# Optimization experiments

Hardware: AMD Instinct MI355X
Metric: run time of the kernel (lower is better)

The kernel has to match this reference:

```python
import jax, jax.numpy as jnp
import numpy as np

N_EMBD = 1024
N_HEAD = 16

def setup_inputs() -> dict:
    key = jax.random.key(0)
    ks = jax.random.split(key, 5)
    x = jax.random.normal(ks[0], (4, 2048, N_EMBD), dtype=jnp.float32)
    # torch Linear default init ~ U(-1/sqrt(fan_in), 1/sqrt(fan_in)); use scaled normals
    s = 1.0 / np.sqrt(N_EMBD)
    W_attn = jax.random.normal(ks[1], (N_EMBD, 3 * N_EMBD), dtype=jnp.float32) * s
    b_attn = jax.random.normal(ks[2], (3 * N_EMBD,), dtype=jnp.float32) * s
    W_proj = jax.random.normal(ks[3], (N_EMBD, N_EMBD), dtype=jnp.float32) * s
    b_proj = jax.random.normal(ks[4], (N_EMBD,), dtype=jnp.float32) * s
    return {"x": x, "W_attn": W_attn, "b_attn": b_attn, "W_proj": W_proj, "b_proj": b_proj}

def reference(x, W_attn, b_attn, W_proj, b_proj) -> jnp.ndarray:
    B, T, C = x.shape
    H = N_HEAD
    D = C // H  # head dim
    qkv = x @ W_attn + b_attn  # [B,T,3C]
    q, k, v = jnp.split(qkv, 3, axis=-1)
    # [B,T,C] -> [B,H,T,D]
    q = q.reshape(B, T, H, D).transpose(0, 2, 1, 3)
    k = k.reshape(B, T, H, D).transpose(0, 2, 1, 3)
    v = v.reshape(B, T, H, D).transpose(0, 2, 1, 3)
    scale = 1.0 / jnp.sqrt(jnp.float32(D))
    att = jnp.einsum('bhqd,bhkd->bhqk', q, k) * scale  # [B,H,T,T]
    causal = jnp.tril(jnp.ones((T, T), dtype=bool))
    att = jnp.where(causal[None, None, :, :], att, -jnp.inf)
    att = jax.nn.softmax(att, axis=-1)
    y = jnp.einsum('bhqk,bhkd->bhqd', att, v)  # [B,H,T,D]
    y = y.transpose(0, 2, 1, 3).reshape(B, T, C)
    return y @ W_proj + b_proj
```

## Files before the change

kernel.cpp:

```cpp
#include <hip/hip_runtime.h>
#include <stdint.h>


typedef __attribute__((ext_vector_type(8))) short short8;
typedef __attribute__((ext_vector_type(4))) float floatx4;

#define AS1C(p) ((const __attribute__((address_space(1))) void*)(p))
#define AS3(p)  ((__attribute__((address_space(3))) void*)(p))

#define SC2F 0.18033688011f

__device__ __forceinline__ unsigned short f2bf(float f) {
  unsigned int u = __builtin_bit_cast(unsigned int, f);
  u = (u + 0x7fffu + ((u >> 16) & 1u)) >> 16;
  return (unsigned short)u;
}
__device__ __forceinline__ unsigned short f2bf_trunc(float f) {
  return (unsigned short)(__builtin_bit_cast(unsigned int, f) >> 16);
}

__global__ void k_cvt(const float* __restrict__ in, unsigned short* __restrict__ out, int n4) {
  int i = blockIdx.x * blockDim.x + threadIdx.x;
  if (i < n4) {
    float4 v = ((const float4*)in)[i];
    ushort4 o;
    o.x = f2bf(v.x); o.y = f2bf(v.y); o.z = f2bf(v.z); o.w = f2bf(v.w);
    ((ushort4*)out)[i] = o;
  }
}

__global__ void k_tw(const float* __restrict__ in, unsigned short* __restrict__ out, int K, int N) {
  __shared__ float t[32][33];
  int n0 = blockIdx.x * 32, k0 = blockIdx.y * 32;
  int tx = threadIdx.x, ty = threadIdx.y;
#pragma unroll
  for (int i = 0; i < 4; i++)
    t[ty + 8 * i][tx] = in[(size_t)(k0 + ty + 8 * i) * N + n0 + tx];
  __syncthreads();
#pragma unroll
  for (int i = 0; i < 4; i++)
    out[(size_t)(n0 + ty + 8 * i) * K + k0 + tx] = f2bf(t[tx][ty + 8 * i]);
}

__global__ void k_tv(const unsigned short* __restrict__ qkv, unsigned short* __restrict__ vt) {
  __shared__ unsigned short t[32][33];
  int t0 = blockIdx.x * 32;
  int d0 = blockIdx.y * 32;
  int bh = blockIdx.z;
  int b = bh >> 4, h = bh & 15;
  int tx = threadIdx.x, ty = threadIdx.y;
#pragma unroll
  for (int i = 0; i < 4; i++)
    t[ty + 8 * i][tx] = qkv[(size_t)(b * 2048 + t0 + ty + 8 * i) * 3072 + 2048 + h * 64 + d0 + tx];
  __syncthreads();
#pragma unroll
  for (int i = 0; i < 4; i++)
    vt[(size_t)(bh * 64 + d0 + ty + 8 * i) * 2048 + t0 + tx] = t[tx][ty + 8 * i];
}

template <int OUT_F32>
__global__ __launch_bounds__(256)
void k_gemm(const unsigned short* __restrict__ A,
            const unsigned short* __restrict__ Bt,
            const float* __restrict__ bias,
            void* __restrict__ Cout, int M, int N, int K, int NX) {
  __shared__ unsigned short lA[128 * 64];
  __shared__ unsigned short lB[128 * 64];
  int lin = blockIdx.x;
  int xcd = lin & 7, idx = lin >> 3;
  int bx = idx % NX;
  int by = xcd + 8 * (idx / NX);
  int tid = threadIdx.x;
  int lane = tid & 63, wv = tid >> 6;
  int lc = lane & 15, quad = lane >> 4;
  int m0 = by * 128, n0 = bx * 128;
  int wm = (wv >> 1) * 64, wn = (wv & 1) * 64;
  int sw = lc & 7;

  floatx4 acc[4][4];
#pragma unroll
  for (int i = 0; i < 4; i++)
#pragma unroll
    for (int j = 0; j < 4; j++) acc[i][j] = (floatx4){0.f, 0.f, 0.f, 0.f};

  int srow = tid >> 3;
  int scol = (((tid & 7) ^ (srow & 7))) * 8;
  const unsigned short* gA = A + (size_t)(m0 + srow) * K + scol;
  const unsigned short* gB = Bt + (size_t)(n0 + srow) * K + scol;

  for (int k0 = 0; k0 < K; k0 += 64) {
#pragma unroll
    for (int c = 0; c < 4; c++) {
      __builtin_amdgcn_global_load_lds(AS1C(gA + (size_t)(32 * c) * K + k0),
                                       AS3(lA + (32 * c + 8 * wv) * 64), 16, 0, 0);
      __builtin_amdgcn_global_load_lds(AS1C(gB + (size_t)(32 * c) * K + k0),
                                       AS3(lB + (32 * c + 8 * wv) * 64), 16, 0, 0);
    }
    __syncthreads();
#pragma unroll
    for (int s = 0; s < 2; s++) {
      short8 af[4], bfr[4];
#pragma unroll
      for (int i = 0; i < 4; i++)
        af[i] = *(const short8*)(lA + (wm + i * 16 + lc) * 64 + (((s * 4 + quad) ^ sw) * 8));
#pragma unroll
      for (int j = 0; j < 4; j++)
        bfr[j] = *(const short8*)(lB + (wn + j * 16 + lc) * 64 + (((s * 4 + quad) ^ sw) * 8));
#pragma unroll
      for (int i = 0; i < 4; i++)
#pragma unroll
        for (int j = 0; j < 4; j++)
          acc[i][j] = __builtin_amdgcn_mfma_f32_16x16x32_bf16(af[i], bfr[j], acc[i][j], 0, 0, 0);
    }
    __syncthreads();
  }

  float bv[4];
#pragma unroll
  for (int j = 0; j < 4; j++) bv[j] = bias[n0 + wn + j * 16 + lc];
#pragma unroll
  for (int i = 0; i < 4; i++) {
#pragma unroll
    for (int j = 0; j < 4; j++) {
      float sc = (!OUT_F32 && (n0 + wn + j * 16) < 1024) ? SC2F : 1.0f;
#pragma unroll
      for (int r = 0; r < 4; r++) {
        size_t idx2 = (size_t)(m0 + wm + i * 16 + quad * 4 + r) * N + (n0 + wn + j * 16 + lc);
        float v = (acc[i][j][r] + bv[j]) * sc;
        if (OUT_F32) ((float*)Cout)[idx2] = v;
        else         ((unsigned short*)Cout)[idx2] = f2bf(v);
      }
    }
  }
}

#define LP_STRIDE 68
__global__ __launch_bounds__(256, 4)
void k_flash(const unsigned short* __restrict__ qkv,
             const unsigned short* __restrict__ vt,
             unsigned short* __restrict__ y) {
  __shared__ unsigned short lK[64 * 64];
  __shared__ unsigned short lVT[64 * 64];
  __shared__ unsigned short lP[4][2][16 * LP_STRIDE];
  int tid = threadIdx.x, lane = tid & 63, wv = tid >> 6;
  int lc = lane & 15, quad = lane >> 4;
  int sw = lc & 7;
  int lin = blockIdx.x;
  int xcd = lin & 7, idx = lin >> 3;
  int j   = idx & 15;
  int bh  = xcd + 8 * (idx >> 4);
  int b = bh >> 4, h = bh & 15;
  int qtA = j, qtB = 31 - j;
  int qrA = qtA * 64 + wv * 16;
  int qrB = qtB * 64 + wv * 16;

  short8 qfA[2], qfB[2];
  {
    const unsigned short* qp = qkv + (size_t)(b * 2048 + qrA + lc) * 3072 + h * 64 + quad * 8;
    qfA[0] = *(const short8*)qp;
    qfA[1] = *(const short8*)(qp + 32);
  }
  {
    const unsigned short* qp = qkv + (size_t)(b * 2048 + qrB + lc) * 3072 + h * 64 + quad * 8;
    qfB[0] = *(const short8*)qp;
    qfB[1] = *(const short8*)(qp + 32);
  }

  float rsA[4] = {0.f, 0.f, 0.f, 0.f}, rsB[4] = {0.f, 0.f, 0.f, 0.f};
  floatx4 oA[4], oB[4];
#pragma unroll
  for (int dt = 0; dt < 4; dt++) {
    oA[dt] = (floatx4){0.f, 0.f, 0.f, 0.f};
    oB[dt] = (floatx4){0.f, 0.f, 0.f, 0.f};
  }

  int srow = tid >> 3;
  int scol = ((tid & 7) ^ (srow & 7)) * 8;
  const unsigned short* gK = qkv + (size_t)(b * 2048 + srow) * 3072 + 1024 + h * 64 + scol;
  const unsigned short* gV = vt + (size_t)(bh * 64 + srow) * 2048 + scol;

  int nt = qtB + 1;

  for (int kv = 0; kv < nt; kv++) {
    int kv0 = kv * 64;
#pragma unroll
    for (int c = 0; c < 2; c++) {
      __builtin_amdgcn_global_load_lds(AS1C(gK + (size_t)(kv0 + 32 * c) * 3072),
                                       AS3(lK + (32 * c + 8 * wv) * 64), 16, 0, 0);
      __builtin_amdgcn_global_load_lds(AS1C(gV + (size_t)(32 * c) * 2048 + kv0),
                                       AS3(lVT + (32 * c + 8 * wv) * 64), 16, 0, 0);
    }
    __syncthreads();

    bool withA = (kv <= qtA);

    floatx4 sB[4], sA[4];
#pragma unroll
    for (int n = 0; n < 4; n++) {
      short8 kf0 = *(const short8*)(lK + (n * 16 + lc) * 64 + ((quad ^ sw) * 8));
      short8 kf1 = *(const short8*)(lK + (n * 16 + lc) * 64 + (((4 + quad) ^ sw) * 8));
      floatx4 t = (floatx4){0.f, 0.f, 0.f, 0.f};
      t = __builtin_amdgcn_mfma_f32_16x16x32_bf16(qfB[0], kf0, t, 0, 0, 0);
      t = __builtin_amdgcn_mfma_f32_16x16x32_bf16(qfB[1], kf1, t, 0, 0, 0);
      sB[n] = t;
      if (withA) {
        floatx4 u = (floatx4){0.f, 0.f, 0.f, 0.f};
        u = __builtin_amdgcn_mfma_f32_16x16x32_bf16(qfA[0], kf0, u, 0, 0, 0);
        u = __builtin_amdgcn_mfma_f32_16x16x32_bf16(qfA[1], kf1, u, 0, 0, 0);
        sA[n] = u;
      }
    }

    {
      bool diag = (kv == qtB);
#pragma unroll
      for (int n = 0; n < 4; n++)
#pragma unroll
        for (int r = 0; r < 4; r++) {
          float arg = sB[n][r];
          if (diag && (kv0 + n * 16 + lc > qrB + quad * 4 + r)) arg = -__builtin_inff();
          float p = __builtin_amdgcn_exp2f(arg);
          rsB[r] += p;
          lP[wv][0][(quad * 4 + r) * LP_STRIDE + n * 16 + lc] = f2bf_trunc(p);
        }
    }
    if (withA) {
      bool diag = (kv == qtA);
#pragma unroll
      for (int n = 0; n < 4; n++)
#pragma unroll
        for (int r = 0; r < 4; r++) {
          float arg = sA[n][r];
          if (diag && (kv0 + n * 16 + lc > qrA + quad * 4 + r)) arg = -__builtin_inff();
          float p = __builtin_amdgcn_exp2f(arg);
          rsA[r] += p;
          lP[wv][1][(quad * 4 + r) * LP_STRIDE + n * 16 + lc] = f2bf_trunc(p);
        }
    }

#pragma unroll
    for (int s2 = 0; s2 < 2; s2++) {
      short8 pfB = *(const short8*)(&lP[wv][0][0] + lc * LP_STRIDE + s2 * 32 + quad * 8);
      short8 pfA;
      if (withA) pfA = *(const short8*)(&lP[wv][1][0] + lc * LP_STRIDE + s2 * 32 + quad * 8);
#pragma unroll
      for (int dt = 0; dt < 4; dt++) {
        short8 vf = *(const short8*)(lVT + (dt * 16 + lc) * 64 + (((s2 * 4 + quad) ^ sw) * 8));
        oB[dt] = __builtin_amdgcn_mfma_f32_16x16x32_bf16(pfB, vf, oB[dt], 0, 0, 0);
        if (withA) oA[dt] = __builtin_amdgcn_mfma_f32_16x16x32_bf16(pfA, vf, oA[dt], 0, 0, 0);
      }
    }
    __syncthreads();
  }

#pragma unroll
  for (int off = 1; off < 16; off <<= 1)
#pragma unroll
    for (int r = 0; r < 4; r++) {
      rsA[r] += __shfl_xor(rsA[r], off);
      rsB[r] += __shfl_xor(rsB[r], off);
    }
#pragma unroll
  for (int r = 0; r < 4; r++) {
    float invA = 1.0f / rsA[r];
    float invB = 1.0f / rsB[r];
#pragma unroll
    for (int dt = 0; dt < 4; dt++) {
      size_t ia = (size_t)(b * 2048 + qrA + quad * 4 + r) * 1024 + h * 64 + dt * 16 + lc;
      size_t ib = (size_t)(b * 2048 + qrB + quad * 4 + r) * 1024 + h * 64 + dt * 16 + lc;
      y[ia] = f2bf(oA[dt][r] * invA);
      y[ib] = f2bf(oB[dt][r] * invB);
    }
  }
}

extern "C" void kernel_launch(void* const* d_in, const int* in_sizes, int n_in,
                              void* d_out, int out_size, void* d_ws, size_t ws_size,
                              hipStream_t stream) {
  const float* x      = (const float*)d_in[0];
  const float* W_attn = (const float*)d_in[1];
  const float* b_attn = (const float*)d_in[2];
  const float* W_proj = (const float*)d_in[3];
  const float* b_proj = (const float*)d_in[4];

  char* ws = (char*)d_ws;
  unsigned short* xb     = (unsigned short*)ws;
  unsigned short* wattnT = (unsigned short*)(ws + 16777216);
  unsigned short* wprojT = (unsigned short*)(ws + 23068672);
  unsigned short* qkv    = (unsigned short*)(ws + 25165824);
  unsigned short* vt     = (unsigned short*)(ws + 75497472);
  unsigned short* y      = xb;

  k_cvt<<<8192, 256, 0, stream>>>(x, xb, 8388608 / 4);
  k_tw<<<dim3(96, 32), dim3(32, 8), 0, stream>>>(W_attn, wattnT, 1024, 3072);
  k_tw<<<dim3(32, 32), dim3(32, 8), 0, stream>>>(W_proj, wprojT, 1024, 1024);
  k_gemm<0><<<24 * 64, 256, 0, stream>>>(xb, wattnT, b_attn, qkv, 8192, 3072, 1024, 24);
  k_tv<<<dim3(64, 2, 64), dim3(32, 8), 0, stream>>>(qkv, vt);
  k_flash<<<1024, 256, 0, stream>>>(qkv, vt, y);
  k_gemm<1><<<8 * 64, 256, 0, stream>>>(y, wprojT, b_proj, d_out, 8192, 1024, 1024, 8);
}
```

Measured before the change: 283.6 us.

## Process four causal-balanced query tiles per flash block sharing K/V loads

Each flash-attention block now handles four query tiles (j, 15-j, 16+j, 31-j) instead of two, so every K/V tile staged in LDS feeds up to four query tiles. This halves the grid to 512 blocks and drops the XCD-aware block remapping in favour of a plain 2D grid. The goal is to cut redundant K/V global loads and barrier overhead per unit of work. In exchange it raises register pressure (four sets of accumulators, with the occupancy hint removed), doubles the P scratch in LDS, and leaves fewer blocks to fill the CUs.

```diff
diff --git a/kernel.cpp b/kernel.cpp
--- a/kernel.cpp
+++ b/kernel.cpp
@@ -135,51 +135,46 @@
 }
 
 #define LP_STRIDE 68
-__global__ __launch_bounds__(256, 4)
+__global__ __launch_bounds__(256)
 void k_flash(const unsigned short* __restrict__ qkv,
              const unsigned short* __restrict__ vt,
              unsigned short* __restrict__ y) {
   __shared__ unsigned short lK[64 * 64];
   __shared__ unsigned short lVT[64 * 64];
-  __shared__ unsigned short lP[4][2][16 * LP_STRIDE];
+  __shared__ unsigned short lP[4][4][16 * LP_STRIDE];
   int tid = threadIdx.x, lane = tid & 63, wv = tid >> 6;
   int lc = lane & 15, quad = lane >> 4;
   int sw = lc & 7;
-  int lin = blockIdx.x;
-  int xcd = lin & 7, idx = lin >> 3;
-  int j   = idx & 15;
-  int bh  = xcd + 8 * (idx >> 4);
+  int j  = blockIdx.x;
+  int bh = blockIdx.y;
   int b = bh >> 4, h = bh & 15;
-  int qtA = j, qtB = 31 - j;
-  int qrA = qtA * 64 + wv * 16;
-  int qrB = qtB * 64 + wv * 16;
-
-  short8 qfA[2], qfB[2];
-  {
-    const unsigned short* qp = qkv + (size_t)(b * 2048 + qrA + lc) * 3072 + h * 64 + quad * 8;
-    qfA[0] = *(const short8*)qp;
-    qfA[1] = *(const short8*)(qp + 32);
-  }
-  {
-    const unsigned short* qp = qkv + (size_t)(b * 2048 + qrB + lc) * 3072 + h * 64 + quad * 8;
-    qfB[0] = *(const short8*)qp;
-    qfB[1] = *(const short8*)(qp + 32);
-  }
-
-  float rsA[4] = {0.f, 0.f, 0.f, 0.f}, rsB[4] = {0.f, 0.f, 0.f, 0.f};
-  floatx4 oA[4], oB[4];
-#pragma unroll
-  for (int dt = 0; dt < 4; dt++) {
-    oA[dt] = (floatx4){0.f, 0.f, 0.f, 0.f};
-    oB[dt] = (floatx4){0.f, 0.f, 0.f, 0.f};
-  }
+  int qt[4] = {j, 15 - j, 16 + j, 31 - j};
+
+  short8 qf[4][2];
+#pragma unroll
+  for (int t = 0; t < 4; t++) {
+    const unsigned short* qp =
+        qkv + (size_t)(b * 2048 + qt[t] * 64 + wv * 16 + lc) * 3072 + h * 64 + quad * 8;
+    qf[t][0] = *(const short8*)qp;
+    qf[t][1] = *(const short8*)(qp + 32);
+  }
+
+  float rs[4][4];
+  floatx4 o[4][4];
+#pragma unroll
+  for (int t = 0; t < 4; t++)
+#pragma unroll
+    for (int r = 0; r < 4; r++) {
+      rs[t][r] = 0.f;
+      o[t][r] = (floatx4){0.f, 0.f, 0.f, 0.f};
+    }
 
   int srow = tid >> 3;
   int scol = ((tid & 7) ^ (srow & 7)) * 8;
   const unsigned short* gK = qkv + (size_t)(b * 2048 + srow) * 3072 + 1024 + h * 64 + scol;
   const unsigned short* gV = vt + (size_t)(bh * 64 + srow) * 2048 + scol;
 
-  int nt = qtB + 1;
+  int nt = 32 - j;
 
   for (int kv = 0; kv < nt; kv++) {
     int kv0 = kv * 64;
@@ -192,86 +187,68 @@
     }
     __syncthreads();
 
-    bool withA = (kv <= qtA);
-
-    floatx4 sB[4], sA[4];
 #pragma unroll
     for (int n = 0; n < 4; n++) {
       short8 kf0 = *(const short8*)(lK + (n * 16 + lc) * 64 + ((quad ^ sw) * 8));
       short8 kf1 = *(const short8*)(lK + (n * 16 + lc) * 64 + (((4 + quad) ^ sw) * 8));
-      floatx4 t = (floatx4){0.f, 0.f, 0.f, 0.f};
-      t = __builtin_amdgcn_mfma_f32_16x16x32_bf16(qfB[0], kf0, t, 0, 0, 0);
-      t = __builtin_amdgcn_mfma_f32_16x16x32_bf16(qfB[1], kf1, t, 0, 0, 0);
-      sB[n] = t;
-      if (withA) {
-        floatx4 u = (floatx4){0.f, 0.f, 0.f, 0.f};
-        u = __builtin_amdgcn_mfma_f32_16x16x32_bf16(qfA[0], kf0, u, 0, 0, 0);
-        u = __builtin_amdgcn_mfma_f32_16x16x32_bf16(qfA[1], kf1, u, 0, 0, 0);
-        sA[n] = u;
-      }
-    }
-
-    {
-      bool diag = (kv == qtB);
-#pragma unroll
-      for (int n = 0; n < 4; n++)
-#pragma unroll
-        for (int r = 0; r < 4; r++) {
-          float arg = sB[n][r];
-          if (diag && (kv0 + n * 16 + lc > qrB + quad * 4 + r)) arg = -__builtin_inff();
-          float p = __builtin_amdgcn_exp2f(arg);
-          rsB[r] += p;
-          lP[wv][0][(quad * 4 + r) * LP_STRIDE + n * 16 + lc] = f2bf_trunc(p);
+#pragma unroll
+      for (int t = 0; t < 4; t++) {
+        if (kv <= qt[t]) {
+          floatx4 s = (floatx4){0.f, 0.f, 0.f, 0.f};
+          s = __builtin_amdgcn_mfma_f32_16x16x32_bf16(qf[t][0], kf0, s, 0, 0, 0);
+          s = __builtin_amdgcn_mfma_f32_16x16x32_bf16(qf[t][1], kf1, s, 0, 0, 0);
+          bool diag = (kv == qt[t]);
+#pragma unroll
+          for (int r = 0; r < 4; r++) {
+            float arg = s[r];
+            if (diag && (n * 16 + lc > wv * 16 + quad * 4 + r)) arg = -__builtin_inff();
+            float p = __builtin_amdgcn_exp2f(arg);
+            rs[t][r] += p;
+            lP[wv][t][(quad * 4 + r) * LP_STRIDE + n * 16 + lc] = f2bf_trunc(p);
+          }
         }
-    }
-    if (withA) {
-      bool diag = (kv == qtA);
-#pragma unroll
-      for (int n = 0; n < 4; n++)
-#pragma unroll
-        for (int r = 0; r < 4; r++) {
-          float arg = sA[n][r];
-          if (diag && (kv0 + n * 16 + lc > qrA + quad * 4 + r)) arg = -__builtin_inff();
-          float p = __builtin_amdgcn_exp2f(arg);
-          rsA[r] += p;
-          lP[wv][1][(quad * 4 + r) * LP_STRIDE + n * 16 + lc] = f2bf_trunc(p);
+      }
+    }
+
+#pragma unroll
+    for (int s2 = 0; s2 < 2; s2++) {
+      short8 vf[4];
+#pragma unroll
+      for (int dt = 0; dt < 4; dt++)
+        vf[dt] = *(const short8*)(lVT + (dt * 16 + lc) * 64 + (((s2 * 4 + quad) ^ sw) * 8));
+#pragma unroll
+      for (int t = 0; t < 4; t++) {
+        if (kv <= qt[t]) {
+          short8 pf = *(const short8*)(&lP[wv][t][0] + lc * LP_STRIDE + s2 * 32 + quad * 8);
+#pragma unroll
+          for (int dt = 0; dt < 4; dt++)
+            o[t][dt] = __builtin_amdgcn_mfma_f32_16x16x32_bf16(pf, vf[dt], o[t][dt], 0, 0, 0);
         }
-    }
-
-#pragma unroll
-    for (int s2 = 0; s2 < 2; s2++) {
-      short8 pfB = *(const short8*)(&lP[wv][0][0] + lc * LP_STRIDE + s2 * 32 + quad * 8);
-      short8 pfA;
-      if (withA) pfA = *(const short8*)(&lP[wv][1][0] + lc * LP_STRIDE + s2 * 32 + quad * 8);
+      }
+    }
+    __syncthreads();
+  }
+
+#pragma unroll
+  for (int off = 1; off < 16; off <<= 1)
+#pragma unroll
+    for (int t = 0; t < 4; t++)
+#pragma unroll
+      for (int r = 0; r < 4; r++)
+        rs[t][r] += __shfl_xor(rs[t][r], off);
+
+#pragma unroll
+  for (int t = 0; t < 4; t++)
+#pragma unroll
+    for (int r = 0; r < 4; r++) {
+      float inv = 1.0f / rs[t][r];
 #pragma unroll
       for (int dt = 0; dt < 4; dt++) {
-        short8 vf = *(const short8*)(lVT + (dt * 16 + lc) * 64 + (((s2 * 4 + quad) ^ sw) * 8));
-        oB[dt] = __builtin_amdgcn_mfma_f32_16x16x32_bf16(pfB, vf, oB[dt], 0, 0, 0);
-        if (withA) oA[dt] = __builtin_amdgcn_mfma_f32_16x16x32_bf16(pfA, vf, oA[dt], 0, 0, 0);
-      }
-    }
-    __syncthreads();
-  }
-
-#pragma unroll
-  for (int off = 1; off < 16; off <<= 1)
-#pragma unroll
-    for (int r = 0; r < 4; r++) {
-      rsA[r] += __shfl_xor(rsA[r], off);
-      rsB[r] += __shfl_xor(rsB[r], off);
-    }
-#pragma unroll
-  for (int r = 0; r < 4; r++) {
-    float invA = 1.0f / rsA[r];
-    float invB = 1.0f / rsB[r];
-#pragma unroll
-    for (int dt = 0; dt < 4; dt++) {
-      size_t ia = (size_t)(b * 2048 + qrA + quad * 4 + r) * 1024 + h * 64 + dt * 16 + lc;
-      size_t ib = (size_t)(b * 2048 + qrB + quad * 4 + r) * 1024 + h * 64 + dt * 16 + lc;
-      y[ia] = f2bf(oA[dt][r] * invA);
-      y[ib] = f2bf(oB[dt][r] * invB);
-    }
-  }
+        size_t ia = (size_t)(b * 2048 + qt[t] * 64 + wv * 16 + quad * 4 + r) * 1024
+                    + h * 64 + dt * 16 + lc;
+        y[ia] = f2bf(o[t][dt][r] * inv);
+      }
+    }
 }
 
 extern "C" void kernel_launch(void* const* d_in, const int* in_sizes, int n_in,
@@ -296,6 +273,6 @@
   k_tw<<<dim3(32, 32), dim3(32, 8), 0, stream>>>(W_proj, wprojT, 1024, 1024);
   k_gemm<0><<<24 * 64, 256, 0, stream>>>(xb, wattnT, b_attn, qkv, 8192, 3072, 1024, 24);
   k_tv<<<dim3(64, 2, 64), dim3(32, 8), 0, stream>>>(qkv, vt);
-  k_flash<<<1024, 256, 0, stream>>>(qkv, vt, y);
+  k_flash<<<dim3(8, 64), 256, 0, stream>>>(qkv, vt, y);
   k_gemm<1><<<8 * 64, 256, 0, stream>>>(y, wprojT, b_proj, d_out, 8192, 1024, 1024, 8);
 }
```

Result: faster. 274.4 us (-3.2%).

## Keep softmax probabilities in registers via transposed QK^T MFMA, drop LDS P staging

Applied to the files above, without the earlier changes.

The flash kernel now computes S^T by swapping the MFMA operands (K as A, Q as B). Each lane then holds four consecutive key positions for one query, which can be packed directly into a bf16 operand for 16x16x16 MFMAs in the PV product. This removes the per-wave LDS round-trip for P and its writes and reads, and simplifies row-sum reduction to two shuffles. It also swaps the XCD-aware 1D block swizzle for a plain 2D grid, which may change L2 locality across XCDs.

```diff
diff --git a/kernel.cpp b/kernel.cpp
--- a/kernel.cpp
+++ b/kernel.cpp
@@ -3,7 +3,9 @@
 
 
 typedef __attribute__((ext_vector_type(8))) short short8;
+typedef __attribute__((ext_vector_type(4))) short short4v;
 typedef __attribute__((ext_vector_type(4))) float floatx4;
+typedef __attribute__((ext_vector_type(2))) unsigned int uint2v;
 
 #define AS1C(p) ((const __attribute__((address_space(1))) void*)(p))
 #define AS3(p)  ((__attribute__((address_space(3))) void*)(p))
@@ -14,9 +16,6 @@
   unsigned int u = __builtin_bit_cast(unsigned int, f);
   u = (u + 0x7fffu + ((u >> 16) & 1u)) >> 16;
   return (unsigned short)u;
-}
-__device__ __forceinline__ unsigned short f2bf_trunc(float f) {
-  return (unsigned short)(__builtin_bit_cast(unsigned int, f) >> 16);
 }
 
 __global__ void k_cvt(const float* __restrict__ in, unsigned short* __restrict__ out, int n4) {
@@ -134,21 +133,17 @@
   }
 }
 
-#define LP_STRIDE 68
 __global__ __launch_bounds__(256, 4)
 void k_flash(const unsigned short* __restrict__ qkv,
              const unsigned short* __restrict__ vt,
              unsigned short* __restrict__ y) {
   __shared__ unsigned short lK[64 * 64];
   __shared__ unsigned short lVT[64 * 64];
-  __shared__ unsigned short lP[4][2][16 * LP_STRIDE];
   int tid = threadIdx.x, lane = tid & 63, wv = tid >> 6;
   int lc = lane & 15, quad = lane >> 4;
   int sw = lc & 7;
-  int lin = blockIdx.x;
-  int xcd = lin & 7, idx = lin >> 3;
-  int j   = idx & 15;
-  int bh  = xcd + 8 * (idx >> 4);
+  int j  = blockIdx.x;
+  int bh = blockIdx.y;
   int b = bh >> 4, h = bh & 15;
   int qtA = j, qtB = 31 - j;
   int qrA = qtA * 64 + wv * 16;
@@ -166,7 +161,7 @@
     qfB[1] = *(const short8*)(qp + 32);
   }
 
-  float rsA[4] = {0.f, 0.f, 0.f, 0.f}, rsB[4] = {0.f, 0.f, 0.f, 0.f};
+  float rsA = 0.f, rsB = 0.f;
   floatx4 oA[4], oB[4];
 #pragma unroll
   for (int dt = 0; dt < 4; dt++) {
@@ -193,84 +188,76 @@
     __syncthreads();
 
     bool withA = (kv <= qtA);
-
-    floatx4 sB[4], sA[4];
+    bool diagA = (kv == qtA), diagB = (kv == qtB);
+
+    short4v pfB[4], pfA[4];
 #pragma unroll
     for (int n = 0; n < 4; n++) {
       short8 kf0 = *(const short8*)(lK + (n * 16 + lc) * 64 + ((quad ^ sw) * 8));
       short8 kf1 = *(const short8*)(lK + (n * 16 + lc) * 64 + (((4 + quad) ^ sw) * 8));
-      floatx4 t = (floatx4){0.f, 0.f, 0.f, 0.f};
-      t = __builtin_amdgcn_mfma_f32_16x16x32_bf16(qfB[0], kf0, t, 0, 0, 0);
-      t = __builtin_amdgcn_mfma_f32_16x16x32_bf16(qfB[1], kf1, t, 0, 0, 0);
-      sB[n] = t;
+      {
+        floatx4 s = (floatx4){0.f, 0.f, 0.f, 0.f};
+        s = __builtin_amdgcn_mfma_f32_16x16x32_bf16(kf0, qfB[0], s, 0, 0, 0);
+        s = __builtin_amdgcn_mfma_f32_16x16x32_bf16(kf1, qfB[1], s, 0, 0, 0);
+        unsigned pu[4];
+#pragma unroll
+        for (int r = 0; r < 4; r++) {
+          float arg = s[r];
+          if (diagB && (n * 16 + quad * 4 + r > wv * 16 + lc)) arg = -__builtin_inff();
+          float p = __builtin_amdgcn_exp2f(arg);
+          rsB += p;
+          pu[r] = __builtin_bit_cast(unsigned, p);
+        }
+        uint2v pk = {(pu[0] >> 16) | (pu[1] & 0xffff0000u),
+                     (pu[2] >> 16) | (pu[3] & 0xffff0000u)};
+        pfB[n] = __builtin_bit_cast(short4v, pk);
+      }
       if (withA) {
-        floatx4 u = (floatx4){0.f, 0.f, 0.f, 0.f};
-        u = __builtin_amdgcn_mfma_f32_16x16x32_bf16(qfA[0], kf0, u, 0, 0, 0);
-        u = __builtin_amdgcn_mfma_f32_16x16x32_bf16(qfA[1], kf1, u, 0, 0, 0);
-        sA[n] = u;
-      }
-    }
-
-    {
-      bool diag = (kv == qtB);
-#pragma unroll
-      for (int n = 0; n < 4; n++)
+        floatx4 s = (floatx4){0.f, 0.f, 0.f, 0.f};
+        s = __builtin_amdgcn_mfma_f32_16x16x32_bf16(kf0, qfA[0], s, 0, 0, 0);
+        s = __builtin_amdgcn_mfma_f32_16x16x32_bf16(kf1, qfA[1], s, 0, 0, 0);
+        unsigned pu[4];
 #pragma unroll
         for (int r = 0; r < 4; r++) {
-          float arg = sB[n][r];
-          if (diag && (kv0 + n * 16 + lc > qrB + quad * 4 + r)) arg = -__builtin_inff();
+          float arg = s[r];
+          if (diagA && (n * 16 + quad * 4 + r > wv * 16 + lc)) arg = -__builtin_inff();
           float p = __builtin_amdgcn_exp2f(arg);
-          rsB[r] += p;
-          lP[wv][0][(quad * 4 + r) * LP_STRIDE + n * 16 + lc] = f2bf_trunc(p);
+          rsA += p;
+          pu[r] = __builtin_bit_cast(unsigned, p);
         }
-    }
-    if (withA) {
-      bool diag = (kv == qtA);
-#pragma unroll
-      for (int n = 0; n < 4; n++)
-#pragma unroll
-        for (int r = 0; r < 4; r++) {
-          float arg = sA[n][r];
-          if (diag && (kv0 + n * 16 + lc > qrA + quad * 4 + r)) arg = -__builtin_inff();
-          float p = __builtin_amdgcn_exp2f(arg);
-          rsA[r] += p;
-          lP[wv][1][(quad * 4 + r) * LP_STRIDE + n * 16 + lc] = f2bf_trunc(p);
-        }
-    }
-
-#pragma unroll
-    for (int s2 = 0; s2 < 2; s2++) {
-      short8 pfB = *(const short8*)(&lP[wv][0][0] + lc * LP_STRIDE + s2 * 32 + quad * 8);
-      short8 pfA;
-      if (withA) pfA = *(const short8*)(&lP[wv][1][0] + lc * LP_STRIDE + s2 * 32 + quad * 8);
+        uint2v pk = {(pu[0] >> 16) | (pu[1] & 0xffff0000u),
+                     (pu[2] >> 16) | (pu[3] & 0xffff0000u)};
+        pfA[n] = __builtin_bit_cast(short4v, pk);
+      }
+    }
+
+#pragma unroll
+    for (int n = 0; n < 4; n++) {
 #pragma unroll
       for (int dt = 0; dt < 4; dt++) {
-        short8 vf = *(const short8*)(lVT + (dt * 16 + lc) * 64 + (((s2 * 4 + quad) ^ sw) * 8));
-        oB[dt] = __builtin_amdgcn_mfma_f32_16x16x32_bf16(pfB, vf, oB[dt], 0, 0, 0);
-        if (withA) oA[dt] = __builtin_amdgcn_mfma_f32_16x16x32_bf16(pfA, vf, oA[dt], 0, 0, 0);
-      }
-    }
-    __syncthreads();
-  }
-
-#pragma unroll
-  for (int off = 1; off < 16; off <<= 1)
-#pragma unroll
-    for (int r = 0; r < 4; r++) {
-      rsA[r] += __shfl_xor(rsA[r], off);
-      rsB[r] += __shfl_xor(rsB[r], off);
-    }
-#pragma unroll
-  for (int r = 0; r < 4; r++) {
-    float invA = 1.0f / rsA[r];
-    float invB = 1.0f / rsB[r];
-#pragma unroll
-    for (int dt = 0; dt < 4; dt++) {
-      size_t ia = (size_t)(b * 2048 + qrA + quad * 4 + r) * 1024 + h * 64 + dt * 16 + lc;
-      size_t ib = (size_t)(b * 2048 + qrB + quad * 4 + r) * 1024 + h * 64 + dt * 16 + lc;
-      y[ia] = f2bf(oA[dt][r] * invA);
-      y[ib] = f2bf(oB[dt][r] * invB);
-    }
+        short4v vf = *(const short4v*)(lVT + (dt * 16 + lc) * 64 +
+                                       (((2 * n + (quad >> 1)) ^ sw) * 8) + (quad & 1) * 4);
+        oB[dt] = __builtin_amdgcn_mfma_f32_16x16x16bf16_1k(vf, pfB[n], oB[dt], 0, 0, 0);
+        if (withA)
+          oA[dt] = __builtin_amdgcn_mfma_f32_16x16x16bf16_1k(vf, pfA[n], oA[dt], 0, 0, 0);
+      }
+    }
+    __syncthreads();
+  }
+
+  rsA += __shfl_xor(rsA, 16); rsA += __shfl_xor(rsA, 32);
+  rsB += __shfl_xor(rsB, 16); rsB += __shfl_xor(rsB, 32);
+  float invA = 1.0f / rsA, invB = 1.0f / rsB;
+
+#pragma unroll
+  for (int dt = 0; dt < 4; dt++) {
+    ushort4 sA, sB;
+    sA.x = f2bf(oA[dt][0] * invA); sA.y = f2bf(oA[dt][1] * invA);
+    sA.z = f2bf(oA[dt][2] * invA); sA.w = f2bf(oA[dt][3] * invA);
+    sB.x = f2bf(oB[dt][0] * invB); sB.y = f2bf(oB[dt][1] * invB);
+    sB.z = f2bf(oB[dt][2] * invB); sB.w = f2bf(oB[dt][3] * invB);
+    *(ushort4*)(y + (size_t)(b * 2048 + qrA + lc) * 1024 + h * 64 + dt * 16 + quad * 4) = sA;
+    *(ushort4*)(y + (size_t)(b * 2048 + qrB + lc) * 1024 + h * 64 + dt * 16 + quad * 4) = sB;
   }
 }
 
@@ -296,6 +283,6 @@
   k_tw<<<dim3(32, 32), dim3(32, 8), 0, stream>>>(W_proj, wprojT, 1024, 1024);
   k_gemm<0><<<24 * 64, 256, 0, stream>>>(xb, wattnT, b_attn, qkv, 8192, 3072, 1024, 24);
   k_tv<<<dim3(64, 2, 64), dim3(32, 8), 0, stream>>>(qkv, vt);
-  k_flash<<<1024, 256, 0, stream>>>(qkv, vt, y);
+  k_flash<<<dim3(16, 64), 256, 0, stream>>>(qkv, vt, y);
   k_gemm<1><<<8 * 64, 256, 0, stream>>>(y, wprojT, b_proj, d_out, 8192, 1024, 1024, 8);
 }
```

Measured after the change: 401.9 us. 41.7% more time.
